# Kernel tuning notes

Hardware: AMD Instinct MI355X
Metric: run time of the kernel (lower is better)

## Reference

```python
import jax, jax.numpy as jnp
import numpy as np

N = 100000
IN_DIM = 256
HID = 128
E = 1600000


def _gcn_conv(x, W, b, src, dst, n_nodes):
    """PyG GCNConv: add self-loops, symmetric normalization, linear transform."""
    xw = x @ W  # [N, H]
    loop = jnp.arange(n_nodes, dtype=src.dtype)
    s = jnp.concatenate([src, loop])  # sources (j)
    d = jnp.concatenate([dst, loop])  # targets (i)
    ones = jnp.ones(s.shape[0], dtype=x.dtype)
    deg = jax.ops.segment_sum(ones, d, num_segments=n_nodes)  # in-degree incl. self-loop
    dinv = jnp.where(deg > 0, jax.lax.rsqrt(deg), 0.0)
    norm = dinv[s] * dinv[d]  # [E+N]
    msgs = xw[s] * norm[:, None]  # gather + scale
    out = jax.ops.segment_sum(msgs, d, num_segments=n_nodes)  # scatter-add at targets
    return out + b


def setup_inputs() -> dict:
    key = jax.random.key(0)
    ks = jax.random.split(key, 12)
    x = jax.random.normal(ks[0], (N, IN_DIM), dtype=jnp.float32)
    edge_index = jax.random.randint(ks[1], (2, E), 0, N, dtype=jnp.int64)
    h_node = jax.random.uniform(ks[2], (N,), dtype=jnp.float32)
    # learned params (glorot-ish scale)
    W1 = jax.random.normal(ks[3], (IN_DIM, HID), dtype=jnp.float32) / np.sqrt(IN_DIM)
    b1 = jnp.zeros((HID,), dtype=jnp.float32)
    W2 = jax.random.normal(ks[4], (HID, HID), dtype=jnp.float32) / np.sqrt(HID)
    b2 = jnp.zeros((HID,), dtype=jnp.float32)
    Wc = jax.random.normal(ks[5], (HID, 2), dtype=jnp.float32) / np.sqrt(HID)
    bc = jnp.zeros((2,), dtype=jnp.float32)
    Wf = jax.random.normal(ks[6], (HID, 2), dtype=jnp.float32) / np.sqrt(HID)
    bf = jnp.zeros((2,), dtype=jnp.float32)
    return {"x": x, "edge_index": edge_index, "h_node": h_node,
            "W1": W1, "b1": b1, "W2": W2, "b2": b2,
            "Wc": Wc, "bc": bc, "Wf": Wf, "bf": bf}


def reference(x, edge_index, h_node, W1, b1, W2, b2, Wc, bc, Wf, bf):
    src, dst = edge_index[0], edge_index[1]
    h1 = jax.nn.relu(_gcn_conv(x, W1, b1, src, dst, x.shape[0]))      # [N, HID]
    logits_coarse = h1 @ Wc + bc                                      # [N, 2]
    alpha = h_node[:, None]                                           # [N, 1]
    h2 = jax.nn.relu(_gcn_conv(h1, W2, b2, src, dst, x.shape[0]))     # [N, HID]
    h2_adaptive = alpha * h2 + (1.0 - alpha) * h1
    logits_fine = h2_adaptive @ Wf + bf                               # [N, 2]
    return 0.5 * logits_coarse + 0.5 * logits_fine
```

## Files before the change

### kernel.cpp

```cpp
#include <hip/hip_runtime.h>


#define HID 128
#define SHIFT 9
#define RANGE 512
#define MAXB 256
#define TILE 4096

typedef __bf16 bf16x8 __attribute__((ext_vector_type(8)));
typedef float  f32x4  __attribute__((ext_vector_type(4)));
typedef float  f32x2  __attribute__((ext_vector_type(2)));

__device__ __forceinline__ unsigned short f2bf(float x) {
    unsigned int b = __float_as_uint(x);
    b += 0x7fffu + ((b >> 16) & 1u);
    return (unsigned short)(b >> 16);
}
__device__ __forceinline__ float bflo(unsigned int u) { return __uint_as_float(u << 16); }
__device__ __forceinline__ float bfhi(unsigned int u) { return __uint_as_float(u & 0xffff0000u); }
__device__ __forceinline__ unsigned packbf(float a, float b) {
    return (unsigned)f2bf(a) | ((unsigned)f2bf(b) << 16);
}


__global__ __launch_bounds__(256)
void bincount_kernel(const int* __restrict__ dst, int* __restrict__ bin_counts,
                     int E, int NB) {
    __shared__ int h[MAXB];
    for (int i = threadIdx.x; i < NB; i += 256) h[i] = 0;
    __syncthreads();
    const int base = blockIdx.x * TILE;
#pragma unroll
    for (int j = 0; j < TILE; j += 256) {
        int e = base + j + threadIdx.x;
        if (e < E) atomicAdd(&h[((unsigned)dst[e]) >> SHIFT], 1);
    }
    __syncthreads();
    for (int i = threadIdx.x; i < NB; i += 256) {
        int v = h[i];
        if (v) atomicAdd(&bin_counts[i], v);
    }
}

__global__ void binscan_kernel(const int* __restrict__ bin_counts,
                               int* __restrict__ bin_off, int* __restrict__ bin_cur, int NB) {
    __shared__ int sh[MAXB];
    const int t = threadIdx.x;
    int v = (t < NB) ? bin_counts[t] : 0;
    sh[t] = v;
    __syncthreads();
    for (int s = 1; s < 256; s <<= 1) {
        int x = (t >= s) ? sh[t - s] : 0;
        __syncthreads();
        sh[t] += x;
        __syncthreads();
    }
    if (t < NB) {
        int ex = sh[t] - v;
        bin_off[t] = ex;
        bin_cur[t] = ex;
    }
}

__global__ __launch_bounds__(256)
void stage_kernel(const int* __restrict__ src, const int* __restrict__ dst,
                  int* __restrict__ bin_cur, unsigned* __restrict__ pairs, int E) {
    __shared__ int sh_hist[MAXB];
    __shared__ int sh_off[MAXB];
    __shared__ int sh_ex[MAXB];
    __shared__ int sh_gbase[MAXB];
    __shared__ uint2 stg[TILE];
    const int t = threadIdx.x;
    const int base = blockIdx.x * TILE;
    const int cnt = min(TILE, E - base);

    for (int i = t; i < MAXB; i += 256) sh_hist[i] = 0;
    __syncthreads();

    int s[16], d[16], r[16];
#pragma unroll
    for (int j = 0; j < 16; ++j) {
        const int k = j * 256 + t;
        if (k < cnt) {
            s[j] = src[base + k];
            d[j] = dst[base + k];
            r[j] = atomicAdd(&sh_hist[((unsigned)d[j]) >> SHIFT], 1);
        }
    }
    __syncthreads();

    const int hv = sh_hist[t];
    sh_off[t] = hv;
    __syncthreads();
    for (int st = 1; st < 256; st <<= 1) {
        int x = (t >= st) ? sh_off[t - st] : 0;
        __syncthreads();
        sh_off[t] += x;
        __syncthreads();
    }
    sh_ex[t] = sh_off[t] - hv;
    if (hv > 0) sh_gbase[t] = atomicAdd(&bin_cur[t], hv);
    __syncthreads();

#pragma unroll
    for (int j = 0; j < 16; ++j) {
        const int k = j * 256 + t;
        if (k < cnt) {
            int b = ((unsigned)d[j]) >> SHIFT;
            stg[sh_ex[b] + r[j]] = make_uint2((unsigned)s[j], (unsigned)d[j]);
        }
    }
    __syncthreads();

    for (int i = t; i < cnt; i += 256) {
        uint2 p = stg[i];
        int b = (int)(p.y >> SHIFT);
        unsigned w = ((p.y & (RANGE - 1)) << 23) | p.x;
        pairs[sh_gbase[b] + (i - sh_ex[b])] = w;
    }
}

__global__ __launch_bounds__(256)
void binrowp_kernel(const unsigned* __restrict__ pairs, const int* __restrict__ bin_off,
                    float* __restrict__ dinv, int* __restrict__ rowp,
                    int N, int NB, int E) {
    __shared__ int c[RANGE];
    __shared__ int sh[256];
    const int b = blockIdx.x;
    const int t = threadIdx.x;
    const int nb = b << SHIFT;
    const int nr = min(RANGE, N - nb);
    for (int i = t; i < RANGE; i += 256) c[i] = 0;
    __syncthreads();
    const int lo = bin_off[b];
    const int hi = (b + 1 < NB) ? bin_off[b + 1] : E;
    for (int i = lo + t; i < hi; i += 256)
        atomicAdd(&c[pairs[i] >> 23], 1);
    __syncthreads();
    const int v0 = c[2 * t], v1 = c[2 * t + 1];
    const int pr = v0 + v1;
    sh[t] = pr;
    __syncthreads();
    for (int s = 1; s < 256; s <<= 1) {
        int x = (t >= s) ? sh[t - s] : 0;
        __syncthreads();
        sh[t] += x;
        __syncthreads();
    }
    const int ex = sh[t] - pr + lo;
    if (2 * t < nr) {
        rowp[nb + 2 * t] = ex;
        dinv[nb + 2 * t] = rsqrtf((float)(v0 + 1));
    }
    if (2 * t + 1 < nr) {
        rowp[nb + 2 * t + 1] = ex + v0;
        dinv[nb + 2 * t + 1] = rsqrtf((float)(v1 + 1));
    }
    if (b == 0 && t == 0) rowp[N] = E;
}

__global__ __launch_bounds__(256)
void fine_kernel(const unsigned* __restrict__ pairs, const int* __restrict__ bin_off,
                 const int* __restrict__ rowp, const float* __restrict__ dinv,
                 unsigned* __restrict__ colv1, int N, int NB, int E) {
    __shared__ int cur[RANGE];
    const int b = blockIdx.x;
    const int nb = b << SHIFT;
    const int nr = min(RANGE, N - nb);
    for (int i = threadIdx.x; i < nr; i += 256) cur[i] = rowp[nb + i];
    __syncthreads();
    const int lo = bin_off[b];
    const int hi = (b + 1 < NB) ? bin_off[b + 1] : E;
    for (int i = lo + threadIdx.x; i < hi; i += 256) {
        unsigned w = pairs[i];
        unsigned s = w & 0x7fffffu;
        int pos = atomicAdd(&cur[w >> 23], 1);
        unsigned w15 = __float2uint_rn(dinv[s] * 32767.0f);
        colv1[pos] = (s << 15) | w15;
    }
}

__global__ void prep_kernel(const float* __restrict__ W1, const float* __restrict__ W2,
                            unsigned short* __restrict__ wt1, unsigned short* __restrict__ wt2,
                            int K1, int* __restrict__ bin_counts) {
    int idx = blockIdx.x * 256 + threadIdx.x;
    if (idx < MAXB) bin_counts[idx] = 0;
    if (idx < 128 * K1) {
        int nn = idx / K1, k = idx - nn * K1;
        wt1[(size_t)nn * K1 + k] = f2bf(W1[(size_t)k * 128 + nn]);
    }
    if (idx < 128 * 128) {
        int nn = idx >> 7, k = idx & 127;
        wt2[(size_t)nn * 128 + k] = f2bf(W2[(size_t)k * 128 + nn]);
    }
}

template <bool A_BF16, int K>
__global__ __launch_bounds__(256)
void gemm_kernel(const void* __restrict__ Aptr, const unsigned short* __restrict__ Wt,
                 unsigned short* __restrict__ Out, int nrows) {
    constexpr int NIT = K / 32;
    constexpr int DEPTH = (NIT < 4) ? NIT : 4;
    const int tid  = threadIdx.x;
    const int wave = tid >> 6;
    const int lane = tid & 63;
    const int q = lane >> 4;
    const int r = lane & 15;
    const int wrow = blockIdx.x * 128 + wave * 32;
    const size_t row0 = (size_t)min(wrow + r,      nrows - 1);
    const size_t row1 = (size_t)min(wrow + 16 + r, nrows - 1);

    const unsigned short* A16 = (const unsigned short*)Aptr;
    const float*          A32 = (const float*)Aptr;

    f32x4 acc[2][8];
#pragma unroll
    for (int s = 0; s < 2; ++s)
#pragma unroll
        for (int c = 0; c < 8; ++c) acc[s][c] = (f32x4){0.f, 0.f, 0.f, 0.f};

    bf16x8 preb[DEPTH][2];
    float4 pref[DEPTH][2][2];

#pragma unroll
    for (int i = 0; i < DEPTH; ++i) {
        const int kk = i * 32 + q * 8;
        if (A_BF16) {
            preb[i][0] = *reinterpret_cast<const bf16x8*>(A16 + row0 * K + kk);
            preb[i][1] = *reinterpret_cast<const bf16x8*>(A16 + row1 * K + kk);
        } else {
            pref[i][0][0] = *reinterpret_cast<const float4*>(A32 + row0 * K + kk);
            pref[i][0][1] = *reinterpret_cast<const float4*>(A32 + row0 * K + kk + 4);
            pref[i][1][0] = *reinterpret_cast<const float4*>(A32 + row1 * K + kk);
            pref[i][1][1] = *reinterpret_cast<const float4*>(A32 + row1 * K + kk + 4);
        }
    }

#pragma unroll
    for (int it = 0; it < NIT; ++it) {
        const int slot = it % DEPTH;
        const int kk = it * 32 + q * 8;

        bf16x8 bfr[8];
#pragma unroll
        for (int c = 0; c < 8; ++c)
            bfr[c] = *reinterpret_cast<const bf16x8*>(Wt + (size_t)(c * 16 + r) * K + kk);

        bf16x8 afrag[2];
#pragma unroll
        for (int s = 0; s < 2; ++s) {
            if (A_BF16) {
                afrag[s] = preb[slot][s];
            } else {
                const float4 x0 = pref[slot][s][0];
                const float4 x1 = pref[slot][s][1];
                bf16x8 a;
                a[0] = (__bf16)x0.x; a[1] = (__bf16)x0.y; a[2] = (__bf16)x0.z; a[3] = (__bf16)x0.w;
                a[4] = (__bf16)x1.x; a[5] = (__bf16)x1.y; a[6] = (__bf16)x1.z; a[7] = (__bf16)x1.w;
                afrag[s] = a;
            }
        }

        if (it + DEPTH < NIT) {
            const int kk2 = (it + DEPTH) * 32 + q * 8;
            if (A_BF16) {
                preb[slot][0] = *reinterpret_cast<const bf16x8*>(A16 + row0 * K + kk2);
                preb[slot][1] = *reinterpret_cast<const bf16x8*>(A16 + row1 * K + kk2);
            } else {
                pref[slot][0][0] = *reinterpret_cast<const float4*>(A32 + row0 * K + kk2);
                pref[slot][0][1] = *reinterpret_cast<const float4*>(A32 + row0 * K + kk2 + 4);
                pref[slot][1][0] = *reinterpret_cast<const float4*>(A32 + row1 * K + kk2);
                pref[slot][1][1] = *reinterpret_cast<const float4*>(A32 + row1 * K + kk2 + 4);
            }
        }

#pragma unroll
        for (int c = 0; c < 8; ++c) {
            acc[0][c] = __builtin_amdgcn_mfma_f32_16x16x32_bf16(afrag[0], bfr[c], acc[0][c], 0, 0, 0);
            acc[1][c] = __builtin_amdgcn_mfma_f32_16x16x32_bf16(afrag[1], bfr[c], acc[1][c], 0, 0, 0);
        }
    }

#pragma unroll
    for (int s = 0; s < 2; ++s)
#pragma unroll
        for (int v = 0; v < 4; ++v) {
            const int row = wrow + s * 16 + q * 4 + v;
            if (row < nrows) {
#pragma unroll
                for (int c = 0; c < 8; ++c)
                    Out[(size_t)row * 128 + c * 16 + r] = f2bf(acc[s][c][v]);
            }
        }
}


#define AGG_EDGE_LOOP(XW)                                                      \
    for (int base = beg; base < end; base += 64) {                             \
        const int e = base + lane;                                             \
        const unsigned cw = (e < end) ? colv1[e] : 0u;                         \
        const int cnt = min(64, end - base);                                   \
        _Pragma("unroll 4")                                                    \
        for (int t = 0; t < cnt; t += 4) {                                     \
            const unsigned cg = (unsigned)__shfl((int)cw, t + q4);             \
            const unsigned st = cg >> 15;                                      \
            const float    wt = (float)(cg & 0x7fffu) * (1.0f / 32767.0f);     \
            const uint4 uu = *reinterpret_cast<const uint4*>(                  \
                (const char*)(XW) + ((st << 8) + coff));                       \
            A0 += (f32x2){bflo(uu.x), bfhi(uu.x)} * wt;                        \
            A1 += (f32x2){bflo(uu.y), bfhi(uu.y)} * wt;                        \
            A2 += (f32x2){bflo(uu.z), bfhi(uu.z)} * wt;                        \
            A3 += (f32x2){bflo(uu.w), bfhi(uu.w)} * wt;                        \
        }                                                                      \
    }                                                                          \
    A0 += __shfl_xor(A0, 16); A1 += __shfl_xor(A1, 16);                        \
    A2 += __shfl_xor(A2, 16); A3 += __shfl_xor(A3, 16);                        \
    A0 += __shfl_xor(A0, 32); A1 += __shfl_xor(A1, 32);                        \
    A2 += __shfl_xor(A2, 32); A3 += __shfl_xor(A3, 32);

__device__ __forceinline__ f32x2 __shfl_xor(f32x2 v, int m) {
    return (f32x2){__shfl_xor(v[0], m), __shfl_xor(v[1], m)};
}

__global__ __launch_bounds__(256)
void agg1_kernel(const unsigned short* __restrict__ xw, const unsigned* __restrict__ colv1,
                 const int* __restrict__ rowp, const float* __restrict__ dinv,
                 const float* __restrict__ b1, const float* __restrict__ Wc,
                 const float* __restrict__ bc, uint4* __restrict__ h1,
                 float* __restrict__ outp, int n) {
    const int node = blockIdx.x * 4 + (threadIdx.x >> 6);
    if (node >= n) return;
    const int lane = threadIdx.x & 63;
    const int c    = lane & 15;
    const int q4   = lane >> 4;
    const unsigned coff = (unsigned)c << 4;
    const float di = dinv[node];

    f32x2 A0 = {0.f,0.f}, A1 = {0.f,0.f}, A2 = {0.f,0.f}, A3 = {0.f,0.f};
    {
        const float ws = (q4 == 0) ? di : 0.f;
        const uint4 uu = *reinterpret_cast<const uint4*>(
            (const char*)xw + (((unsigned)node << 8) + coff));
        A0 += (f32x2){bflo(uu.x), bfhi(uu.x)} * ws;
        A1 += (f32x2){bflo(uu.y), bfhi(uu.y)} * ws;
        A2 += (f32x2){bflo(uu.z), bfhi(uu.z)} * ws;
        A3 += (f32x2){bflo(uu.w), bfhi(uu.w)} * ws;
    }

    const int beg = rowp[node], end = rowp[node + 1];
    AGG_EDGE_LOOP(xw)

    const float4 bb0 = reinterpret_cast<const float4*>(b1)[2*c];
    const float4 bb1 = reinterpret_cast<const float4*>(b1)[2*c + 1];
    float a0 = fmaxf(A0[0]*di + bb0.x, 0.f), a1 = fmaxf(A0[1]*di + bb0.y, 0.f);
    float a2 = fmaxf(A1[0]*di + bb0.z, 0.f), a3 = fmaxf(A1[1]*di + bb0.w, 0.f);
    float a4 = fmaxf(A2[0]*di + bb1.x, 0.f), a5 = fmaxf(A2[1]*di + bb1.y, 0.f);
    float a6 = fmaxf(A3[0]*di + bb1.z, 0.f), a7 = fmaxf(A3[1]*di + bb1.w, 0.f);

    if (q4 == 0)
        h1[((unsigned)node << 4) + c] =
            make_uint4(packbf(a0,a1), packbf(a2,a3), packbf(a4,a5), packbf(a6,a7));

    const float4 w0 = reinterpret_cast<const float4*>(Wc)[4*c];
    const float4 w1 = reinterpret_cast<const float4*>(Wc)[4*c + 1];
    const float4 w2 = reinterpret_cast<const float4*>(Wc)[4*c + 2];
    const float4 w3 = reinterpret_cast<const float4*>(Wc)[4*c + 3];
    float c0 = a0*w0.x + a1*w0.z + a2*w1.x + a3*w1.z
             + a4*w2.x + a5*w2.z + a6*w3.x + a7*w3.z;
    float c1 = a0*w0.y + a1*w0.w + a2*w1.y + a3*w1.w
             + a4*w2.y + a5*w2.w + a6*w3.y + a7*w3.w;
    if (q4) { c0 = 0.f; c1 = 0.f; }
#pragma unroll
    for (int off = 32; off; off >>= 1) {
        c0 += __shfl_down(c0, off);
        c1 += __shfl_down(c1, off);
    }
    if (lane == 0) {
        outp[2 * (size_t)node]     = 0.5f * (c0 + bc[0]);
        outp[2 * (size_t)node + 1] = 0.5f * (c1 + bc[1]);
    }
}

__global__ __launch_bounds__(256)
void agg2_kernel(const unsigned short* __restrict__ xw2, const uint4* __restrict__ h1,
                 const unsigned* __restrict__ colv1, const int* __restrict__ rowp,
                 const float* __restrict__ dinv, const float* __restrict__ b2,
                 const float* __restrict__ Wf, const float* __restrict__ bfv,
                 const float* __restrict__ hnode, float* __restrict__ outp, int n) {
    const int node = blockIdx.x * 4 + (threadIdx.x >> 6);
    if (node >= n) return;
    const int lane = threadIdx.x & 63;
    const int c    = lane & 15;
    const int q4   = lane >> 4;
    const unsigned coff = (unsigned)c << 4;
    const float di = dinv[node];

    f32x2 A0 = {0.f,0.f}, A1 = {0.f,0.f}, A2 = {0.f,0.f}, A3 = {0.f,0.f};
    {
        const float ws = (q4 == 0) ? di : 0.f;
        const uint4 uu = *reinterpret_cast<const uint4*>(
            (const char*)xw2 + (((unsigned)node << 8) + coff));
        A0 += (f32x2){bflo(uu.x), bfhi(uu.x)} * ws;
        A1 += (f32x2){bflo(uu.y), bfhi(uu.y)} * ws;
        A2 += (f32x2){bflo(uu.z), bfhi(uu.z)} * ws;
        A3 += (f32x2){bflo(uu.w), bfhi(uu.w)} * ws;
    }

    const int beg = rowp[node], end = rowp[node + 1];
    AGG_EDGE_LOOP(xw2)

    const float4 bb0 = reinterpret_cast<const float4*>(b2)[2*c];
    const float4 bb1 = reinterpret_cast<const float4*>(b2)[2*c + 1];
    float h20 = fmaxf(A0[0]*di + bb0.x, 0.f), h21 = fmaxf(A0[1]*di + bb0.y, 0.f);
    float h22 = fmaxf(A1[0]*di + bb0.z, 0.f), h23 = fmaxf(A1[1]*di + bb0.w, 0.f);
    float h24 = fmaxf(A2[0]*di + bb1.x, 0.f), h25 = fmaxf(A2[1]*di + bb1.y, 0.f);
    float h26 = fmaxf(A3[0]*di + bb1.z, 0.f), h27 = fmaxf(A3[1]*di + bb1.w, 0.f);

    const float alpha = hnode[node];
    const float beta  = 1.f - alpha;
    const uint4 hh = h1[((unsigned)node << 4) + c];
    const float ha0 = alpha*h20 + beta*bflo(hh.x);
    const float ha1 = alpha*h21 + beta*bfhi(hh.x);
    const float ha2 = alpha*h22 + beta*bflo(hh.y);
    const float ha3 = alpha*h23 + beta*bfhi(hh.y);
    const float ha4 = alpha*h24 + beta*bflo(hh.z);
    const float ha5 = alpha*h25 + beta*bfhi(hh.z);
    const float ha6 = alpha*h26 + beta*bflo(hh.w);
    const float ha7 = alpha*h27 + beta*bfhi(hh.w);

    const float4 w0 = reinterpret_cast<const float4*>(Wf)[4*c];
    const float4 w1 = reinterpret_cast<const float4*>(Wf)[4*c + 1];
    const float4 w2 = reinterpret_cast<const float4*>(Wf)[4*c + 2];
    const float4 w3 = reinterpret_cast<const float4*>(Wf)[4*c + 3];
    float f0 = ha0*w0.x + ha1*w0.z + ha2*w1.x + ha3*w1.z
             + ha4*w2.x + ha5*w2.z + ha6*w3.x + ha7*w3.z;
    float f1 = ha0*w0.y + ha1*w0.w + ha2*w1.y + ha3*w1.w
             + ha4*w2.y + ha5*w2.w + ha6*w3.y + ha7*w3.w;
    if (q4) { f0 = 0.f; f1 = 0.f; }
#pragma unroll
    for (int off = 32; off; off >>= 1) {
        f0 += __shfl_down(f0, off);
        f1 += __shfl_down(f1, off);
    }
    if (lane == 0) {
        outp[2 * (size_t)node]     += 0.5f * (f0 + bfv[0]);
        outp[2 * (size_t)node + 1] += 0.5f * (f1 + bfv[1]);
    }
}


extern "C" void kernel_launch(void* const* d_in, const int* in_sizes, int n_in,
                              void* d_out, int out_size, void* d_ws, size_t ws_size,
                              hipStream_t stream) {
    const float* x     = (const float*)d_in[0];
    const int*   ei    = (const int*)d_in[1];
    const float* hnode = (const float*)d_in[2];
    const float* W1    = (const float*)d_in[3];
    const float* b1    = (const float*)d_in[4];
    const float* W2    = (const float*)d_in[5];
    const float* b2    = (const float*)d_in[6];
    const float* Wc    = (const float*)d_in[7];
    const float* bc    = (const float*)d_in[8];
    const float* Wf    = (const float*)d_in[9];
    const float* bfv   = (const float*)d_in[10];

    const int N  = in_sizes[2];
    const int E  = in_sizes[1] / 2;
    const int K1 = in_sizes[3] / HID;
    const int NB = (N + RANGE - 1) >> SHIFT;
    const int* srcv = ei;
    const int* dstv = ei + E;
    float* outp = (float*)d_out;

    char* ws = (char*)d_ws;
    size_t off = 0;
    auto alloc = [&](size_t bytes) -> char* {
        char* p = ws + off;
        off += (bytes + 255) & ~(size_t)255;
        return p;
    };
    unsigned short* xw       = (unsigned short*)alloc((size_t)N * HID * 2);
    unsigned short* h1       = (unsigned short*)alloc((size_t)N * HID * 2);
    float*          dinv     = (float*)alloc((size_t)N * 4);
    int*            rowp     = (int*)alloc((size_t)(N + 1) * 4);
    unsigned*       colv1    = (unsigned*)alloc((size_t)E * 4);
    unsigned*       pairs    = (unsigned*)alloc((size_t)E * 4);
    int*            bin_counts = (int*)alloc(MAXB * 4);
    int*            bin_off    = (int*)alloc(MAXB * 4);
    int*            bin_cur    = (int*)alloc(MAXB * 4);
    unsigned short* wt1      = (unsigned short*)alloc((size_t)HID * K1 * 2);
    unsigned short* wt2      = (unsigned short*)alloc((size_t)HID * HID * 2);

    prep_kernel<<<(HID * K1 + 255) / 256, 256, 0, stream>>>(W1, W2, wt1, wt2, K1, bin_counts);

    const int ntiles = (E + TILE - 1) / TILE;
    bincount_kernel<<<ntiles, 256, 0, stream>>>(dstv, bin_counts, E, NB);
    binscan_kernel<<<1, 256, 0, stream>>>(bin_counts, bin_off, bin_cur, NB);
    stage_kernel<<<ntiles, 256, 0, stream>>>(srcv, dstv, bin_cur, pairs, E);
    binrowp_kernel<<<NB, 256, 0, stream>>>(pairs, bin_off, dinv, rowp, N, NB, E);
    fine_kernel<<<NB, 256, 0, stream>>>(pairs, bin_off, rowp, dinv, colv1, N, NB, E);

    gemm_kernel<false, 256><<<(N + 127) / 128, 256, 0, stream>>>((const void*)x, wt1, xw, N);
    agg1_kernel<<<(N + 3) / 4, 256, 0, stream>>>(xw, colv1, rowp, dinv,
                                                 b1, Wc, bc, (uint4*)h1, outp, N);
    gemm_kernel<true, 128><<<(N + 127) / 128, 256, 0, stream>>>((const void*)h1, wt2, xw, N);
    agg2_kernel<<<(N + 3) / 4, 256, 0, stream>>>(xw, (const uint4*)h1, colv1,
                                                 rowp, dinv, b2, Wf, bfv, hnode, outp, N);
}
```

Measured before the change: 432.6 us.

## Map one node per 16 lanes and software-pipeline edge gathers in aggregation

```diff
diff --git a/kernel.cpp b/kernel.cpp
--- a/kernel.cpp
+++ b/kernel.cpp
@@ -295,32 +295,42 @@
 }
 
 
-#define AGG_EDGE_LOOP(XW)                                                      \
-    for (int base = beg; base < end; base += 64) {                             \
-        const int e = base + lane;                                             \
-        const unsigned cw = (e < end) ? colv1[e] : 0u;                         \
-        const int cnt = min(64, end - base);                                   \
-        _Pragma("unroll 4")                                                    \
-        for (int t = 0; t < cnt; t += 4) {                                     \
-            const unsigned cg = (unsigned)__shfl((int)cw, t + q4);             \
-            const unsigned st = cg >> 15;                                      \
-            const float    wt = (float)(cg & 0x7fffu) * (1.0f / 32767.0f);     \
-            const uint4 uu = *reinterpret_cast<const uint4*>(                  \
-                (const char*)(XW) + ((st << 8) + coff));                       \
-            A0 += (f32x2){bflo(uu.x), bfhi(uu.x)} * wt;                        \
-            A1 += (f32x2){bflo(uu.y), bfhi(uu.y)} * wt;                        \
-            A2 += (f32x2){bflo(uu.z), bfhi(uu.z)} * wt;                        \
-            A3 += (f32x2){bflo(uu.w), bfhi(uu.w)} * wt;                        \
-        }                                                                      \
-    }                                                                          \
-    A0 += __shfl_xor(A0, 16); A1 += __shfl_xor(A1, 16);                        \
-    A2 += __shfl_xor(A2, 16); A3 += __shfl_xor(A3, 16);                        \
-    A0 += __shfl_xor(A0, 32); A1 += __shfl_xor(A1, 32);                        \
-    A2 += __shfl_xor(A2, 32); A3 += __shfl_xor(A3, 32);
-
-__device__ __forceinline__ f32x2 __shfl_xor(f32x2 v, int m) {
-    return (f32x2){__shfl_xor(v[0], m), __shfl_xor(v[1], m)};
-}
+#define AGG_ISSUE(g, TBL)                                                     \
+    if ((g) * 4 < cnt) {                                                      \
+        _Pragma("unroll")                                                     \
+        for (int j = 0; j < 4; ++j) {                                         \
+            const int sl = (g) * 4 + j;                                       \
+            const unsigned cg = (unsigned)__shfl((int)cw, qb + sl);           \
+            wt[sl] = (float)(cg & 0x7fffu) * (1.0f / 32767.0f);               \
+            pf[sl] = *reinterpret_cast<const uint4*>(                         \
+                (const char*)(TBL) + (((cg >> 15) << 8) + coff));             \
+        }                                                                     \
+    }
+
+#define AGG_CONS(g)                                                          \
+    if ((g) * 4 < cnt) {                                                     \
+        _Pragma("unroll")                                                    \
+        for (int j = 0; j < 4; ++j) {                                        \
+            const int sl = (g) * 4 + j;                                      \
+            const float w = wt[sl];                                          \
+            const uint4 uu = pf[sl];                                         \
+            A0 += (f32x2){bflo(uu.x), bfhi(uu.x)} * w;                       \
+            A1 += (f32x2){bflo(uu.y), bfhi(uu.y)} * w;                       \
+            A2 += (f32x2){bflo(uu.z), bfhi(uu.z)} * w;                       \
+            A3 += (f32x2){bflo(uu.w), bfhi(uu.w)} * w;                       \
+        }                                                                    \
+    }
+
+#define AGG_EDGE_LOOP(TBL)                                                   \
+    unsigned cw = (beg + c < end) ? colv1[beg + c] : 0u;                     \
+    for (int base = beg; base < end; base += 16) {                           \
+        const int cnt = end - base;                                          \
+        AGG_ISSUE(0, TBL) AGG_ISSUE(1, TBL) AGG_ISSUE(2, TBL) AGG_ISSUE(3, TBL) \
+        unsigned cw_next = 0u;                                               \
+        if (base + 16 + c < end) cw_next = colv1[base + 16 + c];             \
+        AGG_CONS(0) AGG_CONS(1) AGG_CONS(2) AGG_CONS(3)                      \
+        cw = cw_next;                                                        \
+    }
 
 __global__ __launch_bounds__(256)
 void agg1_kernel(const unsigned short* __restrict__ xw, const unsigned* __restrict__ colv1,
@@ -328,27 +338,28 @@
                  const float* __restrict__ b1, const float* __restrict__ Wc,
                  const float* __restrict__ bc, uint4* __restrict__ h1,
                  float* __restrict__ outp, int n) {
-    const int node = blockIdx.x * 4 + (threadIdx.x >> 6);
+    const int node = blockIdx.x * 16 + (threadIdx.x >> 4);
     if (node >= n) return;
     const int lane = threadIdx.x & 63;
     const int c    = lane & 15;
-    const int q4   = lane >> 4;
+    const int qb   = lane & 48;
     const unsigned coff = (unsigned)c << 4;
     const float di = dinv[node];
+    const int beg = rowp[node], end = rowp[node + 1];
+
+    const uint4 su = *reinterpret_cast<const uint4*>(
+        (const char*)xw + (((unsigned)node << 8) + coff));
 
     f32x2 A0 = {0.f,0.f}, A1 = {0.f,0.f}, A2 = {0.f,0.f}, A3 = {0.f,0.f};
-    {
-        const float ws = (q4 == 0) ? di : 0.f;
-        const uint4 uu = *reinterpret_cast<const uint4*>(
-            (const char*)xw + (((unsigned)node << 8) + coff));
-        A0 += (f32x2){bflo(uu.x), bfhi(uu.x)} * ws;
-        A1 += (f32x2){bflo(uu.y), bfhi(uu.y)} * ws;
-        A2 += (f32x2){bflo(uu.z), bfhi(uu.z)} * ws;
-        A3 += (f32x2){bflo(uu.w), bfhi(uu.w)} * ws;
-    }
-
-    const int beg = rowp[node], end = rowp[node + 1];
+    uint4 pf[16];
+    float wt[16];
+
     AGG_EDGE_LOOP(xw)
+
+    A0 += (f32x2){bflo(su.x), bfhi(su.x)} * di;
+    A1 += (f32x2){bflo(su.y), bfhi(su.y)} * di;
+    A2 += (f32x2){bflo(su.z), bfhi(su.z)} * di;
+    A3 += (f32x2){bflo(su.w), bfhi(su.w)} * di;
 
     const float4 bb0 = reinterpret_cast<const float4*>(b1)[2*c];
     const float4 bb1 = reinterpret_cast<const float4*>(b1)[2*c + 1];
@@ -357,9 +368,8 @@
     float a4 = fmaxf(A2[0]*di + bb1.x, 0.f), a5 = fmaxf(A2[1]*di + bb1.y, 0.f);
     float a6 = fmaxf(A3[0]*di + bb1.z, 0.f), a7 = fmaxf(A3[1]*di + bb1.w, 0.f);
 
-    if (q4 == 0)
-        h1[((unsigned)node << 4) + c] =
-            make_uint4(packbf(a0,a1), packbf(a2,a3), packbf(a4,a5), packbf(a6,a7));
+    h1[((unsigned)node << 4) + c] =
+        make_uint4(packbf(a0,a1), packbf(a2,a3), packbf(a4,a5), packbf(a6,a7));
 
     const float4 w0 = reinterpret_cast<const float4*>(Wc)[4*c];
     const float4 w1 = reinterpret_cast<const float4*>(Wc)[4*c + 1];
@@ -369,13 +379,12 @@
              + a4*w2.x + a5*w2.z + a6*w3.x + a7*w3.z;
     float c1 = a0*w0.y + a1*w0.w + a2*w1.y + a3*w1.w
              + a4*w2.y + a5*w2.w + a6*w3.y + a7*w3.w;
-    if (q4) { c0 = 0.f; c1 = 0.f; }
-#pragma unroll
-    for (int off = 32; off; off >>= 1) {
-        c0 += __shfl_down(c0, off);
-        c1 += __shfl_down(c1, off);
-    }
-    if (lane == 0) {
+#pragma unroll
+    for (int off = 1; off < 16; off <<= 1) {
+        c0 += __shfl_xor(c0, off);
+        c1 += __shfl_xor(c1, off);
+    }
+    if (c == 0) {
         outp[2 * (size_t)node]     = 0.5f * (c0 + bc[0]);
         outp[2 * (size_t)node + 1] = 0.5f * (c1 + bc[1]);
     }
@@ -387,27 +396,28 @@
                  const float* __restrict__ dinv, const float* __restrict__ b2,
                  const float* __restrict__ Wf, const float* __restrict__ bfv,
                  const float* __restrict__ hnode, float* __restrict__ outp, int n) {
-    const int node = blockIdx.x * 4 + (threadIdx.x >> 6);
+    const int node = blockIdx.x * 16 + (threadIdx.x >> 4);
     if (node >= n) return;
     const int lane = threadIdx.x & 63;
     const int c    = lane & 15;
-    const int q4   = lane >> 4;
+    const int qb   = lane & 48;
     const unsigned coff = (unsigned)c << 4;
     const float di = dinv[node];
+    const int beg = rowp[node], end = rowp[node + 1];
+
+    const uint4 su = *reinterpret_cast<const uint4*>(
+        (const char*)xw2 + (((unsigned)node << 8) + coff));
 
     f32x2 A0 = {0.f,0.f}, A1 = {0.f,0.f}, A2 = {0.f,0.f}, A3 = {0.f,0.f};
-    {
-        const float ws = (q4 == 0) ? di : 0.f;
-        const uint4 uu = *reinterpret_cast<const uint4*>(
-            (const char*)xw2 + (((unsigned)node << 8) + coff));
-        A0 += (f32x2){bflo(uu.x), bfhi(uu.x)} * ws;
-        A1 += (f32x2){bflo(uu.y), bfhi(uu.y)} * ws;
-        A2 += (f32x2){bflo(uu.z), bfhi(uu.z)} * ws;
-        A3 += (f32x2){bflo(uu.w), bfhi(uu.w)} * ws;
-    }
-
-    const int beg = rowp[node], end = rowp[node + 1];
+    uint4 pf[16];
+    float wt[16];
+
     AGG_EDGE_LOOP(xw2)
+
+    A0 += (f32x2){bflo(su.x), bfhi(su.x)} * di;
+    A1 += (f32x2){bflo(su.y), bfhi(su.y)} * di;
+    A2 += (f32x2){bflo(su.z), bfhi(su.z)} * di;
+    A3 += (f32x2){bflo(su.w), bfhi(su.w)} * di;
 
     const float4 bb0 = reinterpret_cast<const float4*>(b2)[2*c];
     const float4 bb1 = reinterpret_cast<const float4*>(b2)[2*c + 1];
@@ -436,13 +446,12 @@
              + ha4*w2.x + ha5*w2.z + ha6*w3.x + ha7*w3.z;
     float f1 = ha0*w0.y + ha1*w0.w + ha2*w1.y + ha3*w1.w
              + ha4*w2.y + ha5*w2.w + ha6*w3.y + ha7*w3.w;
-    if (q4) { f0 = 0.f; f1 = 0.f; }
-#pragma unroll
-    for (int off = 32; off; off >>= 1) {
-        f0 += __shfl_down(f0, off);
-        f1 += __shfl_down(f1, off);
-    }
-    if (lane == 0) {
+#pragma unroll
+    for (int off = 1; off < 16; off <<= 1) {
+        f0 += __shfl_xor(f0, off);
+        f1 += __shfl_xor(f1, off);
+    }
+    if (c == 0) {
         outp[2 * (size_t)node]     += 0.5f * (f0 + bfv[0]);
         outp[2 * (size_t)node + 1] += 0.5f * (f1 + bfv[1]);
     }
@@ -501,9 +510,9 @@
     fine_kernel<<<NB, 256, 0, stream>>>(pairs, bin_off, rowp, dinv, colv1, N, NB, E);
 
     gemm_kernel<false, 256><<<(N + 127) / 128, 256, 0, stream>>>((const void*)x, wt1, xw, N);
-    agg1_kernel<<<(N + 3) / 4, 256, 0, stream>>>(xw, colv1, rowp, dinv,
-                                                 b1, Wc, bc, (uint4*)h1, outp, N);
+    agg1_kernel<<<(N + 15) / 16, 256, 0, stream>>>(xw, colv1, rowp, dinv,
+                                                   b1, Wc, bc, (uint4*)h1, outp, N);
     gemm_kernel<true, 128><<<(N + 127) / 128, 256, 0, stream>>>((const void*)h1, wt2, xw, N);
-    agg2_kernel<<<(N + 3) / 4, 256, 0, stream>>>(xw, (const uint4*)h1, colv1,
-                                                 rowp, dinv, b2, Wf, bfv, hnode, outp, N);
-}
+    agg2_kernel<<<(N + 15) / 16, 256, 0, stream>>>(xw, (const uint4*)h1, colv1,
+                                                   rowp, dinv, b2, Wf, bfv, hnode, outp, N);
+}
```

Measured after the change: 402.6 us. -6.9%, faster.
